# Optimization experiments

Measured on AMD Instinct MI355X. Metric: run time of the kernel, lower is better.

The kernel has to match this reference:

```python
import jax, jax.numpy as jnp
import numpy as np

B, S, E, H = 8, 1024, 768, 12
D = E // H  # per-head dim


def setup_inputs() -> dict:
    key = jax.random.key(0)
    ks = jax.random.split(key, 9)
    glorot = lambda k: jax.random.normal(k, (E, E), jnp.float32) * np.sqrt(2.0 / (E + E))
    return {
        "inputs": jax.random.normal(ks[0], (B, S, E), jnp.float32),
        "Wq": glorot(ks[1]), "bq": jnp.zeros((E,), jnp.float32),
        "Wk": glorot(ks[2]), "bk": jnp.zeros((E,), jnp.float32),
        "Wv": glorot(ks[3]), "bv": jnp.zeros((E,), jnp.float32),
        "Wo": glorot(ks[4]), "bo": jnp.zeros((E,), jnp.float32),
    }


def reference(inputs, Wq, bq, Wk, bk, Wv, bv, Wo, bo):
    b, s, e = inputs.shape
    # QKV projections then split heads: [B,S,E] -> [B,H,S,D]
    def heads(x):
        return x.reshape(b, s, H, D).transpose(0, 2, 1, 3)
    q = heads(inputs @ Wq + bq)
    k = heads(inputs @ Wk + bk)
    v = heads(inputs @ Wv + bv)
    scale = 1.0 / jnp.sqrt(jnp.asarray(D, inputs.dtype))
    scores = jnp.einsum("bhqd,bhkd->bhqk", q, k) * scale
    weights = jax.nn.softmax(scores, axis=-1)  # attn_drop rate 0 -> identity
    attn = jnp.einsum("bhqk,bhkd->bhqd", weights, v)
    concat = attn.transpose(0, 2, 1, 3).reshape(b, s, e)
    out = concat @ Wo + bo  # proj_drop rate 0 -> identity
    return out
```

## Files before the change

### kernel.cpp

```cpp
#include <hip/hip_runtime.h>
#include <math.h>

#define BB 8
#define SS 1024
#define EE 768
#define HH 12
#define DD 64
#define MM (BB*SS)

typedef __attribute__((ext_vector_type(8))) short short8;
typedef __attribute__((ext_vector_type(4))) short short4v;
typedef __attribute__((ext_vector_type(4))) float f32x4;
typedef __attribute__((ext_vector_type(4))) int int4v;

static __device__ __forceinline__ short f2bf(float x) {
    unsigned u = __float_as_uint(x);
    u += 0x7fffu + ((u >> 16) & 1u);
    return (short)(u >> 16);
}
static __device__ __forceinline__ short f2bf_fast(float x) {
    return (short)((__float_as_uint(x) + 0x8000u) >> 16);
}

static __device__ __forceinline__ int cvtpk_bf16(float lo, float hi) {
    int r;
    asm("v_cvt_pk_bf16_f32 %0, %1, %2" : "=v"(r) : "v"(lo), "v"(hi));
    return r;
}
static __device__ __forceinline__ short8 i4_to_s8(int4v v) {
    union { int4v i; short8 s; } u; u.i = v; return u.s;
}

static __device__ __forceinline__ void gload_lds16(const void* g, void* l) {
    __builtin_amdgcn_global_load_lds((__attribute__((address_space(1))) void*)g,
                                     (__attribute__((address_space(3))) void*)l,
                                     16, 0, 0);
}

#define BAR __builtin_amdgcn_s_barrier()
#define VMW(n) asm volatile("s_waitcnt vmcnt(" #n ")" ::: "memory")

__global__ __launch_bounds__(256)
void prep(const float* __restrict__ X, short* __restrict__ Xb,
          const float* __restrict__ W0, const float* __restrict__ W1,
          const float* __restrict__ W2, const float* __restrict__ W3,
          short* __restrict__ Wt) {
    const int tid = threadIdx.x;
    if (blockIdx.x < 6144) {
        const long i = ((long)blockIdx.x * 256 + tid) * 4;
        float4 v = *(const float4*)&X[i];
        short4v o;
        o.x = f2bf(v.x); o.y = f2bf(v.y); o.z = f2bf(v.z); o.w = f2bf(v.w);
        *(short4v*)&Xb[i] = o;
        return;
    }
    __shared__ short T[64][72];
    const int id = blockIdx.x - 6144;
    const int z  = id / 144;
    const int r2 = id % 144;
    const int i0 = (r2 / 12) * 64;
    const int j0 = (r2 % 12) * 64;
    const float* sp = (z == 0) ? W0 : (z == 1) ? W1 : (z == 2) ? W2 : W3;
    short* dp = Wt + (long)z * EE * EE;
#pragma unroll
    for (int rep = 0; rep < 4; ++rep) {
        const int r = (tid >> 4) + rep * 16;
        const int c = (tid & 15) * 4;
        float4 v = *(const float4*)&sp[(long)(i0 + r) * EE + j0 + c];
        T[c + 0][r] = f2bf(v.x);
        T[c + 1][r] = f2bf(v.y);
        T[c + 2][r] = f2bf(v.z);
        T[c + 3][r] = f2bf(v.w);
    }
    __syncthreads();
#pragma unroll
    for (int rep = 0; rep < 4; ++rep) {
        const int rr = (tid >> 4) + rep * 16;
        const int cc = (tid & 15) * 4;
        short4v o;
        o.x = T[rr][cc + 0]; o.y = T[rr][cc + 1];
        o.z = T[rr][cc + 2]; o.w = T[rr][cc + 3];
        *(short4v*)&dp[(long)(j0 + rr) * EE + i0 + cc] = o;
    }
}

#define GEMM_CORE(Abase, Bbase, row0, col0)                                     \
    f32x4 acc[4][4];                                                            \
    _Pragma("unroll") for (int i = 0; i < 4; ++i)                               \
        _Pragma("unroll") for (int j = 0; j < 4; ++j)                           \
            acc[i][j] = (f32x4){0.f, 0.f, 0.f, 0.f};                            \
    const int rm = (w & 1) * 64, cn = (w >> 1) * 64;                            \
    for (int k0 = 0; k0 < EE; k0 += 64) {                                       \
        __syncthreads();                                                        \
        _Pragma("unroll") for (int i = 0; i < 4; ++i) {                         \
            const int chunk = w * 256 + i * 64 + lane;                          \
            const int r = chunk >> 3;                                          \
            const int cs = (((chunk & 7) ^ (r & 7)) << 3);                      \
            short* ldsA = Al + (w * 256 + i * 64) * 8;                          \
            short* ldsB = Bl + (w * 256 + i * 64) * 8;                          \
            gload_lds16(&Abase[(long)(row0 + r) * EE + k0 + cs], ldsA);         \
            gload_lds16(&Bbase[(long)(col0 + r) * EE + k0 + cs], ldsB);         \
        }                                                                       \
        __syncthreads();                                                        \
        _Pragma("unroll") for (int ks = 0; ks < 2; ++ks) {                      \
            short8 af[4], bf[4];                                                \
            _Pragma("unroll") for (int t = 0; t < 4; ++t)                       \
                af[t] = *(const short8*)&Al[(rm + t * 16 + m) * 64 +            \
                                            (((ks * 4 + quad) ^ (m & 7)) << 3)]; \
            _Pragma("unroll") for (int t = 0; t < 4; ++t)                       \
                bf[t] = *(const short8*)&Bl[(cn + t * 16 + m) * 64 +            \
                                            (((ks * 4 + quad) ^ (m & 7)) << 3)]; \
            _Pragma("unroll") for (int mt = 0; mt < 4; ++mt)                    \
                _Pragma("unroll") for (int nt = 0; nt < 4; ++nt)                \
                    acc[mt][nt] = __builtin_amdgcn_mfma_f32_16x16x32_bf16(      \
                        af[mt], bf[nt], acc[mt][nt], 0, 0, 0);                  \
        }                                                                       \
    }

#define QSCALE 0.1803368801111204f

#define STG1(Ld, Gbase, gr0, k0)                                              \
    do {                                                                      \
        const int r_ = tid >> 3;                                              \
        const int cs_ = ((tid & 7) ^ (r_ & 7)) << 3;                          \
        gload_lds16(&(Gbase)[(long)((gr0) + r_) * EE + (k0) + cs_],           \
                    (Ld) + w * 512);                                          \
    } while (0)

#define QKV_RDA(Ld, mb)                                                       \
    _Pragma("unroll") for (int t = 0; t < 4; ++t)                             \
        _Pragma("unroll") for (int ks = 0; ks < 2; ++ks)                      \
            af[t][ks] = *(const short8*)&(Ld)[(wr * 128 + ((mb) + t) * 16 + m) * 64 + \
                                              (((ks * 4 + quad) ^ (m & 7)) << 3)];

#define QKV_RDB(Ld)                                                           \
    _Pragma("unroll") for (int t = 0; t < 2; ++t)                             \
        _Pragma("unroll") for (int ks = 0; ks < 2; ++ks)                      \
            bf[t][ks] = *(const short8*)&(Ld)[(wc * 32 + t * 16 + m) * 64 +   \
                                              (((ks * 4 + quad) ^ (m & 7)) << 3)];

#define QKV_MF(mb)                                                            \
    __builtin_amdgcn_s_setprio(1);                                            \
    _Pragma("unroll") for (int mq = 0; mq < 4; ++mq)                          \
        _Pragma("unroll") for (int nq = 0; nq < 2; ++nq)                      \
            _Pragma("unroll") for (int ks = 0; ks < 2; ++ks)                  \
                acc[(mb) + mq][nq] = __builtin_amdgcn_mfma_f32_16x16x32_bf16( \
                    af[mq][ks], bf[nq][ks], acc[(mb) + mq][nq], 0, 0, 0);     \
    __builtin_amdgcn_s_setprio(0);

__global__ __launch_bounds__(512, 2)
void gemm_qkv(const short* __restrict__ Xb, const short* __restrict__ Wt,
              const float* __restrict__ bq, const float* __restrict__ bk,
              const float* __restrict__ bv,
              short* __restrict__ Qb, short* __restrict__ Kb,
              short* __restrict__ Vb) {
    __shared__ short SMEM[40960];
    short* const Ae = SMEM;
    short* const Ao = SMEM + 16384;
    short* const Bl = SMEM + 32768;

    const int tid = threadIdx.x;
    const int w = tid >> 6;
    const int m = tid & 15, quad = (tid & 63) >> 4;
    const int wr = w >> 2, wc = w & 3;

    const int flat = blockIdx.x + 18 * blockIdx.y;
    const int id   = (flat & 7) * 72 + (flat >> 3);
    const int lcl  = id % 72;
    const int rt   = (id / 72) * 4 + (lcl & 3);
    const int ct   = lcl >> 2;
    const int row0 = rt * 256;
    const int wsel = ct / 6;
    const int col0w = (ct % 6) * 128;
    const short* Wsel = Wt + (long)wsel * EE * EE;
    const float* bias = (wsel == 0) ? bq : (wsel == 1) ? bk : bv;

    f32x4 acc[8][2];
#pragma unroll
    for (int i = 0; i < 8; ++i)
#pragma unroll
        for (int j = 0; j < 2; ++j) acc[i][j] = (f32x4){0.f, 0.f, 0.f, 0.f};

    STG1(Ae + 0,     Xb,   row0 + 0,    0);
    STG1(Ae + 8192,  Xb,   row0 + 128,  0);
    STG1(Ae + 4096,  Xb,   row0 + 64,   0);
    STG1(Ae + 12288, Xb,   row0 + 192,  0);
    STG1(Bl + 0,     Wsel, col0w + 0,   0);
    STG1(Bl + 4096,  Wsel, col0w + 64,  0);
    STG1(Ao + 0,     Xb,   row0 + 0,    64);
    STG1(Ao + 8192,  Xb,   row0 + 128,  64);
    VMW(2);
    BAR;

#pragma unroll 1
    for (int it = 0; it < 6; ++it) {
        const int kO1 = (2 * it + 1) * 64;
        const int t2 = 2 * it + 2, t3 = 2 * it + 3;
        const int kE2 = (t2 < 12 ? t2 : 11) * 64;
        const int kO3 = (t3 < 12 ? t3 : 11) * 64;
        short8 af[4][2], bf[2][2];
        QKV_RDA(Ae, 0);
        QKV_RDB(Bl);
        STG1(Ao + 4096,  Xb, row0 + 64,  kO1);
        STG1(Ao + 12288, Xb, row0 + 192, kO1);
        BAR;
        QKV_MF(0);
        BAR;
        QKV_RDA(Ae, 4);
        STG1(Bl + 0,     Wsel, col0w + 0,  kO1);
        STG1(Bl + 4096,  Wsel, col0w + 64, kO1);
        STG1(Ae + 0,     Xb,   row0 + 0,   kE2);
        STG1(Ae + 8192,  Xb,   row0 + 128, kE2);
        BAR;
        QKV_MF(4);
        VMW(2);
        BAR;
        QKV_RDA(Ao, 0);
        QKV_RDB(Bl);
        STG1(Ae + 4096,  Xb, row0 + 64,  kE2);
        STG1(Ae + 12288, Xb, row0 + 192, kE2);
        BAR;
        QKV_MF(0);
        BAR;
        QKV_RDA(Ao, 4);
        STG1(Bl + 0,     Wsel, col0w + 0,  kE2);
        STG1(Bl + 4096,  Wsel, col0w + 64, kE2);
        STG1(Ao + 0,     Xb,   row0 + 0,   kO3);
        STG1(Ao + 8192,  Xb,   row0 + 128, kO3);
        BAR;
        QKV_MF(4);
        VMW(2);
        BAR;
    }

    VMW(0);
    __syncthreads();
    const int b = row0 >> 10, s0 = row0 & 1023;
    short* EP = SMEM;

    if (wsel < 2) {
        const float scale = (wsel == 0) ? QSCALE : 1.0f;
        short* QK = (wsel == 0) ? Qb : Kb;
#pragma unroll
        for (int nt = 0; nt < 2; ++nt) {
            const float bvv = bias[col0w + wc * 32 + nt * 16 + m];
#pragma unroll
            for (int mt = 0; mt < 8; ++mt)
#pragma unroll
                for (int r = 0; r < 4; ++r)
                    EP[(wr * 128 + mt * 16 + quad * 4 + r) * 136 + wc * 32 + nt * 16 + m] =
                        f2bf((acc[mt][nt][r] + bvv) * scale);
        }
        __syncthreads();
#pragma unroll
        for (int rep = 0; rep < 8; ++rep) {
            const int chunk = tid + rep * 512;
            const int row = chunk >> 4;
            const int cc = (chunk & 15) * 8;
            const int colg = col0w + cc;
            const int h = colg >> 6, d = colg & 63;
            short8 v = *(const short8*)&EP[row * 136 + cc];
            *(short8*)&QK[((long)(b * HH + h) * SS + s0 + row) * DD + d] = v;
        }
    } else {
#pragma unroll
        for (int nt = 0; nt < 2; ++nt) {
            const float bvv = bias[col0w + wc * 32 + nt * 16 + m];
#pragma unroll
            for (int mt = 0; mt < 8; ++mt) {
                short4v o;
                o.x = f2bf(acc[mt][nt][0] + bvv);
                o.y = f2bf(acc[mt][nt][1] + bvv);
                o.z = f2bf(acc[mt][nt][2] + bvv);
                o.w = f2bf(acc[mt][nt][3] + bvv);
                *(short4v*)&EP[(wc * 32 + nt * 16 + m) * 264 + wr * 128 + mt * 16 + quad * 4] = o;
            }
        }
        __syncthreads();
#pragma unroll
        for (int rep = 0; rep < 8; ++rep) {
            const int chunk = tid + rep * 512;
            const int col = chunk >> 5;
            const int sc8 = (chunk & 31) * 8;
            const int colg = col0w + col;
            const int h = colg >> 6, d = colg & 63;
            short8 v = *(const short8*)&EP[col * 264 + sc8];
            *(short8*)&Vb[((long)(b * HH + h) * DD + d) * SS + s0 + sc8] = v;
        }
    }
}

__global__ __launch_bounds__(256)
void gemm_proj(const short* __restrict__ Cb, const short* __restrict__ WoT,
               const float* __restrict__ bo, float* __restrict__ out) {
    __shared__ short Al[128 * 64];
    __shared__ short Bl[128 * 64];
    const int tid = threadIdx.x, w = tid >> 6, lane = tid & 63;
    const int m = lane & 15, quad = lane >> 4;

    const int flat = blockIdx.x + 6 * blockIdx.y;
    const int id   = (flat & 7) * 48 + (flat >> 3);
    const int xcd  = id / 48;
    const int lcl  = id % 48;
    const int row0 = (xcd * 8 + (lcl & 7)) * 128;
    const int col0 = (lcl >> 3) * 128;

    GEMM_CORE(Cb, WoT, row0, col0)

#pragma unroll
    for (int nt = 0; nt < 4; ++nt) {
        const int colg = col0 + cn + nt * 16 + m;
        const float bvv = bo[colg];
#pragma unroll
        for (int mt = 0; mt < 4; ++mt)
#pragma unroll
            for (int r = 0; r < 4; ++r) {
                const int srow = row0 + rm + mt * 16 + quad * 4 + r;
                out[(long)srow * EE + colg] = acc[mt][nt][r] + bvv;
            }
    }
}

#define ATTN_STAGE(Kdst, Vdst, k0)                                            \
    do {                                                                      \
        _Pragma("unroll") for (int i = 0; i < 2; ++i) {                       \
            const int chunk = w * 128 + i * 64 + l;                           \
            const int r = chunk >> 3;                                         \
            const int cs = ((chunk & 7) ^ (r & 7)) << 3;                      \
            gload_lds16(&Kg[(long)((k0) + r) * DD + cs],                      \
                        (Kdst) + (w * 128 + i * 64) * 8);                     \
            gload_lds16(&Vg[(long)r * SS + (k0) + cs],                        \
                        (Vdst) + (w * 128 + i * 64) * 8);                     \
        }                                                                     \
    } while (0)

#define ATTN_COMPUTE(Kbuf, Vbuf)                                              \
    do {                                                                      \
        f32x4 sc[2][4];                                                       \
        __builtin_amdgcn_s_setprio(1);                                        \
        _Pragma("unroll") for (int nt = 0; nt < 4; ++nt) {                    \
            const short* kb = (Kbuf) + (nt * 16 + m) * 64;                    \
            short8 a0 = *(const short8*)&kb[(quad ^ (m & 7)) << 3];           \
            short8 a1 = *(const short8*)&kb[((4 + quad) ^ (m & 7)) << 3];     \
            _Pragma("unroll") for (int g = 0; g < 2; ++g) {                   \
                f32x4 a = (f32x4){0.f, 0.f, 0.f, 0.f};                        \
                a = __builtin_amdgcn_mfma_f32_16x16x32_bf16(a0, aq[g][0], a, 0, 0, 0); \
                a = __builtin_amdgcn_mfma_f32_16x16x32_bf16(a1, aq[g][1], a, 0, 0, 0); \
                sc[g][nt] = a;                                                \
            }                                                                 \
        }                                                                     \
        __builtin_amdgcn_s_setprio(0);                                        \
        _Pragma("unroll") for (int g = 0; g < 2; ++g)                         \
            _Pragma("unroll") for (int nt = 0; nt < 4; ++nt)                  \
                _Pragma("unroll") for (int r = 0; r < 4; ++r)                 \
                    sc[g][nt][r] = __builtin_amdgcn_exp2f(sc[g][nt][r]);      \
        short8 ap[2][2];                                                      \
        _Pragma("unroll") for (int g = 0; g < 2; ++g)                         \
            _Pragma("unroll") for (int hf = 0; hf < 2; ++hf) {                \
                int4v wv;                                                     \
                wv.x = cvtpk_bf16(sc[g][2 * hf + 0][0], sc[g][2 * hf + 0][1]); \
                wv.y = cvtpk_bf16(sc[g][2 * hf + 0][2], sc[g][2 * hf + 0][3]); \
                wv.z = cvtpk_bf16(sc[g][2 * hf + 1][0], sc[g][2 * hf + 1][1]); \
                wv.w = cvtpk_bf16(sc[g][2 * hf + 1][2], sc[g][2 * hf + 1][3]); \
                ap[g][hf] = i4_to_s8(wv);                                     \
            }                                                                 \
        __builtin_amdgcn_s_setprio(1);                                        \
        _Pragma("unroll") for (int g = 0; g < 2; ++g) {                       \
            lacc[g] = __builtin_amdgcn_mfma_f32_16x16x32_bf16(ap[g][0], ones, lacc[g], 0, 0, 0); \
            lacc[g] = __builtin_amdgcn_mfma_f32_16x16x32_bf16(ap[g][1], ones, lacc[g], 0, 0, 0); \
        }                                                                     \
        const int rsw = m & 7, hb = (quad & 1) * 4;                           \
        _Pragma("unroll") for (int dt = 0; dt < 4; ++dt) {                    \
            const short* vb = (Vbuf) + (dt * 16 + m) * 64;                    \
            short4v l0 = *(const short4v*)&vb[((((quad >> 1) + 0) ^ rsw) << 3) + hb]; \
            short4v h0 = *(const short4v*)&vb[((((quad >> 1) + 2) ^ rsw) << 3) + hb]; \
            short4v l1 = *(const short4v*)&vb[((((quad >> 1) + 4) ^ rsw) << 3) + hb]; \
            short4v h1 = *(const short4v*)&vb[((((quad >> 1) + 6) ^ rsw) << 3) + hb]; \
            short8 b0 = __builtin_shufflevector(l0, h0, 0, 1, 2, 3, 4, 5, 6, 7); \
            short8 b1 = __builtin_shufflevector(l1, h1, 0, 1, 2, 3, 4, 5, 6, 7); \
            _Pragma("unroll") for (int g = 0; g < 2; ++g) {                   \
                O[g][dt] = __builtin_amdgcn_mfma_f32_16x16x32_bf16(ap[g][0], b0, O[g][dt], 0, 0, 0); \
                O[g][dt] = __builtin_amdgcn_mfma_f32_16x16x32_bf16(ap[g][1], b1, O[g][dt], 0, 0, 0); \
            }                                                                 \
        }                                                                     \
        __builtin_amdgcn_s_setprio(0);                                        \
    } while (0)

__global__ __launch_bounds__(256)
void attn_mfma(const short* __restrict__ Q,
               const short* __restrict__ K,
               const short* __restrict__ Vt,
               short* __restrict__ out) {
    __shared__ short K0l[64 * 64];
    __shared__ short K1l[64 * 64];
    __shared__ short V0l[64 * 64];
    __shared__ short V1l[64 * 64];

    const int tid  = threadIdx.x;
    const int w    = tid >> 6;
    const int l    = tid & 63;
    const int m    = l & 15;
    const int quad = l >> 4;

    const int flat = blockIdx.x + 8 * blockIdx.y + 96 * blockIdx.z;
    const int id   = (flat & 7) * 96 + (flat >> 3);
    const int qt   = id & 7;
    const int bh   = id >> 3;
    const int b    = bh / HH;
    const int h    = bh % HH;
    const int q0   = qt * 128;

    const short* Qg = Q  + (long)bh * SS * DD;
    const short* Kg = K  + (long)bh * SS * DD;
    const short* Vg = Vt + (long)bh * DD * SS;

    short8 aq[2][2];
#pragma unroll
    for (int g = 0; g < 2; ++g) {
        const int row = q0 + w * 32 + g * 16 + m;
        aq[g][0] = *(const short8*)(Qg + (long)row * DD + quad * 8);
        aq[g][1] = *(const short8*)(Qg + (long)row * DD + 32 + quad * 8);
    }

    short8 ones;
#pragma unroll
    for (int i = 0; i < 8; ++i) ones[i] = (short)0x3F80;

    f32x4 O[2][4], lacc[2];
#pragma unroll
    for (int g = 0; g < 2; ++g) {
        lacc[g] = (f32x4){0.f, 0.f, 0.f, 0.f};
#pragma unroll
        for (int dt = 0; dt < 4; ++dt) O[g][dt] = (f32x4){0.f, 0.f, 0.f, 0.f};
    }

    ATTN_STAGE(K0l, V0l, 0);
    __syncthreads();

#pragma unroll 1
    for (int kt2 = 0; kt2 < 8; ++kt2) {
        const int k0 = kt2 * 128;
        ATTN_STAGE(K1l, V1l, k0 + 64);
        ATTN_COMPUTE(K0l, V0l);
        __syncthreads();
        if (kt2 < 7) ATTN_STAGE(K0l, V0l, k0 + 128);
        ATTN_COMPUTE(K1l, V1l);
        __syncthreads();
    }

#pragma unroll
    for (int g = 0; g < 2; ++g)
#pragma unroll
        for (int r = 0; r < 4; ++r) {
            const float inv = 1.0f / lacc[g][r];
            const int qo = q0 + w * 32 + g * 16 + quad * 4 + r;
            short* orow = out + ((long)(b * SS + qo)) * EE + h * DD;
#pragma unroll
            for (int dt = 0; dt < 4; ++dt)
                orow[dt * 16 + m] = f2bf(O[g][dt][r] * inv);
        }
}

extern "C" void kernel_launch(void* const* d_in, const int* in_sizes, int n_in,
                              void* d_out, int out_size, void* d_ws, size_t ws_size,
                              hipStream_t stream) {
    const float* X  = (const float*)d_in[0];
    const float* Wq = (const float*)d_in[1];
    const float* bq = (const float*)d_in[2];
    const float* Wk = (const float*)d_in[3];
    const float* bk = (const float*)d_in[4];
    const float* Wv = (const float*)d_in[5];
    const float* bv = (const float*)d_in[6];
    const float* Wo = (const float*)d_in[7];
    const float* bo = (const float*)d_in[8];

    const long SEG = (long)BB * HH * SS * DD;
    const long WSEG = (long)EE * EE;
    short* Xb = (short*)d_ws;
    short* Wt = Xb + SEG;
    short* Qb = Wt + 4 * WSEG;
    short* Kb = Qb + SEG;
    short* Vb = Kb + SEG;
    short* Cb = Vb + SEG;

    prep<<<dim3(6720), 256, 0, stream>>>(X, Xb, Wq, Wk, Wv, Wo, Wt);

    gemm_qkv<<<dim3(18, 32), 512, 0, stream>>>(Xb, Wt, bq, bk, bv, Qb, Kb, Vb);

    attn_mfma<<<dim3(SS / 128, HH, BB), 256, 0, stream>>>(Qb, Kb, Vb, Cb);

    gemm_proj<<<dim3(6, 64), 256, 0, stream>>>(Cb, Wt + 3 * WSEG, bo,
                                               (float*)d_out);
}
```

Before: 196.7 us.

## Shrink QKV GEMM LDS with rotating three-buffer A staging and split epilogue

Replaces the double-buffered full A tiles (Ae/Ao, 32K shorts) with three rotating half-tile buffers, cutting shared memory from 80KB to 64KB per block. The epilogue is split into two passes, one per wave-row half, so the staging area fits in the smaller LDS footprint. The goal is to keep two 512-thread blocks resident per CU under the LDS limit, or to free LDS, while keeping the loads pipelined. In exchange the epilogue gets extra barriers and serialization, and the buffer rotation changes the prefetch distance and wait points.

```diff
diff --git a/kernel.cpp b/kernel.cpp
--- a/kernel.cpp
+++ b/kernel.cpp
@@ -127,10 +127,10 @@
                     (Ld) + w * 512);                                          \
     } while (0)
 
-#define QKV_RDA(Ld, mb)                                                       \
+#define QKV_RDA3(Sl)                                                          \
     _Pragma("unroll") for (int t = 0; t < 4; ++t)                             \
         _Pragma("unroll") for (int ks = 0; ks < 2; ++ks)                      \
-            af[t][ks] = *(const short8*)&(Ld)[(wr * 128 + ((mb) + t) * 16 + m) * 64 + \
+            af[t][ks] = *(const short8*)&(Sl)[wr * 4096 + (t * 16 + m) * 64 + \
                                               (((ks * 4 + quad) ^ (m & 7)) << 3)];
 
 #define QKV_RDB(Ld)                                                           \
@@ -154,10 +154,8 @@
               const float* __restrict__ bv,
               short* __restrict__ Qb, short* __restrict__ Kb,
               short* __restrict__ Vb) {
-    __shared__ short SMEM[40960];
-    short* const Ae = SMEM;
-    short* const Ao = SMEM + 16384;
-    short* const Bl = SMEM + 32768;
+    __shared__ short SMEM[32768];
+    short* const Bl = SMEM + 24576;
 
     const int tid = threadIdx.x;
     const int w = tid >> 6;
@@ -181,56 +179,60 @@
 #pragma unroll
         for (int j = 0; j < 2; ++j) acc[i][j] = (f32x4){0.f, 0.f, 0.f, 0.f};
 
-    STG1(Ae + 0,     Xb,   row0 + 0,    0);
-    STG1(Ae + 8192,  Xb,   row0 + 128,  0);
-    STG1(Ae + 4096,  Xb,   row0 + 64,   0);
-    STG1(Ae + 12288, Xb,   row0 + 192,  0);
-    STG1(Bl + 0,     Wsel, col0w + 0,   0);
-    STG1(Bl + 4096,  Wsel, col0w + 64,  0);
-    STG1(Ao + 0,     Xb,   row0 + 0,    64);
-    STG1(Ao + 8192,  Xb,   row0 + 128,  64);
+    short* SA = SMEM;
+    short* SB = SMEM + 8192;
+    short* SC = SMEM + 16384;
+
+    STG1(SA + 0,    Xb,   row0 + 0,    0);
+    STG1(SA + 4096, Xb,   row0 + 128,  0);
+    STG1(Bl + 0,    Wsel, col0w + 0,   0);
+    STG1(Bl + 4096, Wsel, col0w + 64,  0);
+    STG1(SB + 0,    Xb,   row0 + 64,   0);
+    STG1(SB + 4096, Xb,   row0 + 192,  0);
     VMW(2);
     BAR;
 
 #pragma unroll 1
     for (int it = 0; it < 6; ++it) {
         const int kO1 = (2 * it + 1) * 64;
-        const int t2 = 2 * it + 2, t3 = 2 * it + 3;
+        const int t2 = 2 * it + 2;
         const int kE2 = (t2 < 12 ? t2 : 11) * 64;
-        const int kO3 = (t3 < 12 ? t3 : 11) * 64;
         short8 af[4][2], bf[2][2];
-        QKV_RDA(Ae, 0);
+        QKV_RDA3(SA);
         QKV_RDB(Bl);
-        STG1(Ao + 4096,  Xb, row0 + 64,  kO1);
-        STG1(Ao + 12288, Xb, row0 + 192, kO1);
+        STG1(SC + 0,    Xb, row0 + 0,   kO1);
+        STG1(SC + 4096, Xb, row0 + 128, kO1);
         BAR;
         QKV_MF(0);
-        BAR;
-        QKV_RDA(Ae, 4);
-        STG1(Bl + 0,     Wsel, col0w + 0,  kO1);
-        STG1(Bl + 4096,  Wsel, col0w + 64, kO1);
-        STG1(Ae + 0,     Xb,   row0 + 0,   kE2);
-        STG1(Ae + 8192,  Xb,   row0 + 128, kE2);
+        VMW(2);
+        BAR;
+        QKV_RDA3(SB);
+        STG1(Bl + 0,    Wsel, col0w + 0,  kO1);
+        STG1(Bl + 4096, Wsel, col0w + 64, kO1);
+        STG1(SA + 0,    Xb,   row0 + 64,  kO1);
+        STG1(SA + 4096, Xb,   row0 + 192, kO1);
         BAR;
         QKV_MF(4);
         VMW(2);
         BAR;
-        QKV_RDA(Ao, 0);
+        QKV_RDA3(SC);
         QKV_RDB(Bl);
-        STG1(Ae + 4096,  Xb, row0 + 64,  kE2);
-        STG1(Ae + 12288, Xb, row0 + 192, kE2);
+        STG1(SB + 0,    Xb, row0 + 0,   kE2);
+        STG1(SB + 4096, Xb, row0 + 128, kE2);
         BAR;
         QKV_MF(0);
-        BAR;
-        QKV_RDA(Ao, 4);
-        STG1(Bl + 0,     Wsel, col0w + 0,  kE2);
-        STG1(Bl + 4096,  Wsel, col0w + 64, kE2);
-        STG1(Ao + 0,     Xb,   row0 + 0,   kO3);
-        STG1(Ao + 8192,  Xb,   row0 + 128, kO3);
+        VMW(2);
+        BAR;
+        QKV_RDA3(SA);
+        STG1(Bl + 0,    Wsel, col0w + 0,  kE2);
+        STG1(Bl + 4096, Wsel, col0w + 64, kE2);
+        STG1(SC + 0,    Xb,   row0 + 64,  kE2);
+        STG1(SC + 4096, Xb,   row0 + 192, kE2);
         BAR;
         QKV_MF(4);
         VMW(2);
         BAR;
+        short* tmp = SA; SA = SB; SB = SC; SC = tmp;
     }
 
     VMW(0);
@@ -241,51 +243,63 @@
     if (wsel < 2) {
         const float scale = (wsel == 0) ? QSCALE : 1.0f;
         short* QK = (wsel == 0) ? Qb : Kb;
-#pragma unroll
-        for (int nt = 0; nt < 2; ++nt) {
-            const float bvv = bias[col0w + wc * 32 + nt * 16 + m];
-#pragma unroll
-            for (int mt = 0; mt < 8; ++mt)
-#pragma unroll
-                for (int r = 0; r < 4; ++r)
-                    EP[(wr * 128 + mt * 16 + quad * 4 + r) * 136 + wc * 32 + nt * 16 + m] =
-                        f2bf((acc[mt][nt][r] + bvv) * scale);
-        }
-        __syncthreads();
-#pragma unroll
-        for (int rep = 0; rep < 8; ++rep) {
-            const int chunk = tid + rep * 512;
-            const int row = chunk >> 4;
-            const int cc = (chunk & 15) * 8;
-            const int colg = col0w + cc;
-            const int h = colg >> 6, d = colg & 63;
-            short8 v = *(const short8*)&EP[row * 136 + cc];
-            *(short8*)&QK[((long)(b * HH + h) * SS + s0 + row) * DD + d] = v;
+#pragma unroll 1
+        for (int hh = 0; hh < 2; ++hh) {
+            if (wr == hh) {
+#pragma unroll
+                for (int nt = 0; nt < 2; ++nt) {
+                    const float bvv = bias[col0w + wc * 32 + nt * 16 + m];
+#pragma unroll
+                    for (int mt = 0; mt < 8; ++mt)
+#pragma unroll
+                        for (int r = 0; r < 4; ++r)
+                            EP[(mt * 16 + quad * 4 + r) * 136 + wc * 32 + nt * 16 + m] =
+                                f2bf((acc[mt][nt][r] + bvv) * scale);
+                }
+            }
+            __syncthreads();
+#pragma unroll
+            for (int rep = 0; rep < 4; ++rep) {
+                const int chunk = tid + rep * 512;
+                const int row = chunk >> 4;
+                const int cc = (chunk & 15) * 8;
+                const int colg = col0w + cc;
+                const int h = colg >> 6, d = colg & 63;
+                short8 v = *(const short8*)&EP[row * 136 + cc];
+                *(short8*)&QK[((long)(b * HH + h) * SS + s0 + hh * 128 + row) * DD + d] = v;
+            }
+            __syncthreads();
         }
     } else {
-#pragma unroll
-        for (int nt = 0; nt < 2; ++nt) {
-            const float bvv = bias[col0w + wc * 32 + nt * 16 + m];
-#pragma unroll
-            for (int mt = 0; mt < 8; ++mt) {
-                short4v o;
-                o.x = f2bf(acc[mt][nt][0] + bvv);
-                o.y = f2bf(acc[mt][nt][1] + bvv);
-                o.z = f2bf(acc[mt][nt][2] + bvv);
-                o.w = f2bf(acc[mt][nt][3] + bvv);
-                *(short4v*)&EP[(wc * 32 + nt * 16 + m) * 264 + wr * 128 + mt * 16 + quad * 4] = o;
+#pragma unroll 1
+        for (int hh = 0; hh < 2; ++hh) {
+            if (wr == hh) {
+#pragma unroll
+                for (int nt = 0; nt < 2; ++nt) {
+                    const float bvv = bias[col0w + wc * 32 + nt * 16 + m];
+#pragma unroll
+                    for (int mt = 0; mt < 8; ++mt) {
+                        short4v o;
+                        o.x = f2bf(acc[mt][nt][0] + bvv);
+                        o.y = f2bf(acc[mt][nt][1] + bvv);
+                        o.z = f2bf(acc[mt][nt][2] + bvv);
+                        o.w = f2bf(acc[mt][nt][3] + bvv);
+                        *(short4v*)&EP[(wc * 32 + nt * 16 + m) * 136 + mt * 16 + quad * 4] = o;
+                    }
+                }
             }
-        }
-        __syncthreads();
-#pragma unroll
-        for (int rep = 0; rep < 8; ++rep) {
-            const int chunk = tid + rep * 512;
-            const int col = chunk >> 5;
-            const int sc8 = (chunk & 31) * 8;
-            const int colg = col0w + col;
-            const int h = colg >> 6, d = colg & 63;
-            short8 v = *(const short8*)&EP[col * 264 + sc8];
-            *(short8*)&Vb[((long)(b * HH + h) * DD + d) * SS + s0 + sc8] = v;
+            __syncthreads();
+#pragma unroll
+            for (int rep = 0; rep < 4; ++rep) {
+                const int chunk = tid + rep * 512;
+                const int col = chunk >> 4;
+                const int sc8 = (chunk & 15) * 8;
+                const int colg = col0w + col;
+                const int h = colg >> 6, d = colg & 63;
+                short8 v = *(const short8*)&EP[col * 136 + sc8];
+                *(short8*)&Vb[((long)(b * HH + h) * DD + d) * SS + s0 + hh * 128 + sc8] = v;
+            }
+            __syncthreads();
         }
     }
 }
```

New measurement: 200.3 us. About the same (+1.8%).
